# Kernel tuning notes

Measured on AMD Instinct MI355X. Metric: run time of the kernel, lower is better.

## Reference

```python
import jax, jax.numpy as jnp
import numpy as np
from math import sqrt

D_MODEL = 1024
N_HEADS = 16
FFN = 4096
B, N = 2, 2048
EPS = 1e-5


def _layernorm(x, g, b):
    mu = jnp.mean(x, -1, keepdims=True)
    var = jnp.mean((x - mu) ** 2, -1, keepdims=True)
    return (x - mu) * jax.lax.rsqrt(var + EPS) * g + b


def setup_inputs() -> dict:
    key = jax.random.key(0)
    ks = jax.random.split(key, 12)
    s = 1.0 / sqrt(D_MODEL)
    sf = 1.0 / sqrt(FFN)
    inp = {
        "tgt": jax.random.normal(ks[0], (B, N, D_MODEL), jnp.float32),
        # True = masked. Causal: query i may attend to keys j <= i.
        "tgt_mask": jnp.triu(jnp.ones((N, N), jnp.bool_), k=1),
        "tgt_key_pad_mask": jnp.zeros((B, N), jnp.bool_),
        "Wq": jax.random.uniform(ks[1], (D_MODEL, D_MODEL), jnp.float32, -s, s),
        "Wk": jax.random.uniform(ks[2], (D_MODEL, D_MODEL), jnp.float32, -s, s),
        "Wv": jax.random.uniform(ks[3], (D_MODEL, D_MODEL), jnp.float32, -s, s),
        "Wo": jax.random.uniform(ks[4], (D_MODEL, D_MODEL), jnp.float32, -s, s),
        "bo": jax.random.uniform(ks[5], (D_MODEL,), jnp.float32, -s, s),
        "W1": jax.random.uniform(ks[6], (FFN, D_MODEL), jnp.float32, -s, s),
        "b1": jax.random.uniform(ks[7], (FFN,), jnp.float32, -s, s),
        "W2": jax.random.uniform(ks[8], (D_MODEL, FFN), jnp.float32, -sf, sf),
        "b2": jax.random.uniform(ks[9], (D_MODEL,), jnp.float32, -sf, sf),
        "g1": jnp.ones((D_MODEL,), jnp.float32),
        "beta1": jnp.zeros((D_MODEL,), jnp.float32),
        "g2": jnp.ones((D_MODEL,), jnp.float32),
        "beta2": jnp.zeros((D_MODEL,), jnp.float32),
    }
    return inp


def _mha(x, tgt_mask, pad_mask, Wq, Wk, Wv, Wo, bo):
    b, n, d = x.shape
    dk = d // N_HEADS
    q = (x @ Wq.T).reshape(b, n, N_HEADS, dk).transpose(0, 2, 1, 3)  # bhnd
    k = (x @ Wk.T).reshape(b, n, N_HEADS, dk).transpose(0, 2, 1, 3)
    v = (x @ Wv.T).reshape(b, n, N_HEADS, dk).transpose(0, 2, 1, 3)
    scores = jnp.einsum("bhqd,bhkd->bhqk", q, k) / sqrt(dk)
    mask = tgt_mask[None, None, :, :] | pad_mask[:, None, None, :]
    scores = jnp.where(mask, -jnp.inf, scores)
    att = jax.nn.softmax(scores, axis=-1)
    out = jnp.einsum("bhqk,bhkd->bhqd", att, v).transpose(0, 2, 1, 3).reshape(b, n, d)
    return out @ Wo.T + bo


def reference(tgt, tgt_mask, tgt_key_pad_mask, Wq, Wk, Wv, Wo, bo,
              W1, b1, W2, b2, g1, beta1, g2, beta2):
    # PostNorm logic (pre_norm=False), dropout=0 (eval)
    h = _mha(tgt, tgt_mask, tgt_key_pad_mask, Wq, Wk, Wv, Wo, bo)
    x = _layernorm(tgt + h, g1, beta1)
    m = jax.nn.gelu(x @ W1.T + b1, approximate=True) @ W2.T + b2
    return _layernorm(x + m, g2, beta2)
```

## Files before the change

kernel.cpp:

```cpp
#include <hip/hip_runtime.h>


#define DEV __device__ __forceinline__

typedef __attribute__((ext_vector_type(4)))  float f32x4;
typedef __attribute__((ext_vector_type(16))) float f32x16;
typedef __attribute__((ext_vector_type(8)))  short s16x8;

static constexpr int Bb   = 2;
static constexpr int NN   = 2048;
static constexpr int DM   = 1024;
static constexpr int HH   = 16;
static constexpr int DK   = 64;
static constexpr int FF   = 4096;
static constexpr int ROWS = Bb * NN;

#define AS1(p) ((const __attribute__((address_space(1))) void*)(p))
#define AS3(p) ((__attribute__((address_space(3))) void*)(p))

DEV unsigned short f2bf(float f) {
  unsigned u = __float_as_uint(f);
  u += 0x7fff + ((u >> 16) & 1);
  return (unsigned short)(u >> 16);
}
DEV float fexp2(float x) {
  float r;
  asm("v_exp_f32 %0, %1" : "=v"(r) : "v"(x));
  return r;
}
DEV unsigned cvtpk(float lo, float hi) {
  unsigned r;
  asm("v_cvt_pk_bf16_f32 %0, %1, %2" : "=v"(r) : "v"(lo), "v"(hi));
  return r;
}

__global__ __launch_bounds__(256) void k_cast(const float* __restrict__ in,
                                              ushort* __restrict__ out, int n4) {
  int i = blockIdx.x * 256 + threadIdx.x;
  if (i >= n4) return;
  float4 v = reinterpret_cast<const float4*>(in)[i];
  ushort4 o;
  o.x = f2bf(v.x); o.y = f2bf(v.y); o.z = f2bf(v.z); o.w = f2bf(v.w);
  reinterpret_cast<ushort4*>(out)[i] = o;
}

template <int EPI, int BN, bool QKV>
__global__ __launch_bounds__(256) void k_gemm(
    const ushort* __restrict__ A, const ushort* __restrict__ Bt,
    const float* __restrict__ bias, const float* __restrict__ resid,
    ushort* __restrict__ Cb, float* __restrict__ Cf,
    int K, int nbx) {
  __shared__ ushort As[2][128][32];
  __shared__ ushort Bs[2][BN][32];

  const int t = threadIdx.x;
  const int lane = t & 63, w = t >> 6;
  const int lr = lane & 15, lg = lane >> 4;
  const int lrow = lane >> 2, lc8 = (lane & 3) * 8;

  const int nwg = gridDim.x;
  const int bid = blockIdx.x;
  const int q8 = nwg >> 3, r8 = nwg & 7;
  const int xcd = bid & 7, lin = bid >> 3;
  const int wg = (xcd < r8 ? xcd * (q8 + 1) : r8 * (q8 + 1) + (xcd - r8) * q8) + lin;
  const int band = wg / (4 * nbx);
  const int inn  = wg % (4 * nbx);
  const int by = band * 4 + (inn & 3);
  const int bx = inn >> 2;

  const int bRow = by * 128;
  const int bCol = bx * BN;

  constexpr int NW = BN / 32;
  const int wRow = (w >> 1) * 64, wCol = (w & 1) * (BN / 2);

  const f32x4 zero = {0.f, 0.f, 0.f, 0.f};
  f32x4 acc[4][NW];
#pragma unroll
  for (int m = 0; m < 4; ++m)
#pragma unroll
    for (int n = 0; n < NW; ++n) acc[m][n] = zero;

  auto stage = [&](int buf, int kt) {
#pragma unroll
    for (int i = 0; i < 2; ++i) {
      int rr = w * 32 + i * 16;
      __builtin_amdgcn_global_load_lds(
          AS1(A + (size_t)(bRow + rr + lrow) * K + kt + lc8),
          AS3(&As[buf][rr][0]), 16, 0, 0);
    }
#pragma unroll
    for (int i = 0; i < BN / 64; ++i) {
      int rr = w * (BN / 4) + i * 16;
      __builtin_amdgcn_global_load_lds(
          AS1(Bt + (size_t)(bCol + rr + lrow) * K + kt + lc8),
          AS3(&Bs[buf][rr][0]), 16, 0, 0);
    }
  };

  stage(0, 0);
  const int nk = K / 32;
  for (int tt = 0; tt < nk; ++tt) {
    const int cur = tt & 1;
    __syncthreads();
    if (tt + 1 < nk) stage(cur ^ 1, (tt + 1) * 32);

    s16x8 af[4], bfr[NW];
#pragma unroll
    for (int m = 0; m < 4; ++m)
      af[m] = *reinterpret_cast<const s16x8*>(&As[cur][wRow + m * 16 + lr][lg * 8]);
#pragma unroll
    for (int n = 0; n < NW; ++n)
      bfr[n] = *reinterpret_cast<const s16x8*>(&Bs[cur][wCol + n * 16 + lr][lg * 8]);
#pragma unroll
    for (int m = 0; m < 4; ++m)
#pragma unroll
      for (int n = 0; n < NW; ++n)
        acc[m][n] = __builtin_amdgcn_mfma_f32_16x16x32_bf16(af[m], bfr[n], acc[m][n], 0, 0, 0);
  }

  ushort* CbOut = Cb;
  int colBase = bCol, Ncols = nbx * BN, third = 0;
  if (QKV) {
    third = bCol >> 10;
    CbOut = Cb + (size_t)third * ROWS * DM;
    colBase = bCol & 1023;
    Ncols = DM;
  }
#pragma unroll
  for (int m = 0; m < 4; ++m) {
    int gr = bRow + wRow + m * 16 + lg * 4;
#pragma unroll
    for (int n = 0; n < NW; ++n) {
      int gc = colBase + wCol + n * 16 + lr;
      float bv = (EPI == 1 || EPI == 2) ? bias[gc] : 0.0f;
#pragma unroll
      for (int r = 0; r < 4; ++r) {
        int nr = gr + r;
        float v = acc[m][n][r] + bv;
        if (EPI == 2) {
          size_t idx = (size_t)nr * Ncols + gc;
          Cf[idx] = v + resid[idx];
        } else if (EPI == 1) {
          size_t idx = (size_t)nr * Ncols + gc;
          float u = v + 0.044715f * v * v * v;
          float g = v / (1.0f + __expf(-1.5957691216057308f * u));
          CbOut[idx] = f2bf(g);
        } else {
          int gcs = gc;
          if (QKV && third == 1)
            gcs = (gc & ~63) | ((gc ^ ((nr & 7) << 3)) & 63);
          CbOut[(size_t)nr * Ncols + gcs] = f2bf(v);
        }
      }
    }
  }
}

__global__ __launch_bounds__(256) void k_vt(const ushort* __restrict__ V,
                                            ushort* __restrict__ vT) {
  __shared__ ushort Ls[64][72];
  const int t = threadIdx.x;
  const int n0 = blockIdx.x * 64;
  const int bh = blockIdx.y;
  const int b = bh >> 4, h = bh & 15;
  const int n = t >> 2;
#pragma unroll
  for (int half = 0; half < 2; ++half) {
    int c8 = ((t & 3) + half * 4) * 8;
    int4 v = *reinterpret_cast<const int4*>(
        V + ((size_t)(b * NN + n0 + n)) * DM + h * DK + c8);
    *reinterpret_cast<int4*>(&Ls[n][c8]) = v;
  }
  __syncthreads();
  const int d = t >> 2;
#pragma unroll
  for (int half = 0; half < 2; ++half) {
    int c = (t & 3) + half * 4;
    ushort tmp[8];
#pragma unroll
    for (int j = 0; j < 8; ++j) tmp[j] = Ls[c * 8 + j][d];
    size_t out = ((size_t)bh * DK + d) * NN + n0 + ((c ^ (d & 7)) * 8);
    *reinterpret_cast<int4*>(vT + out) = *reinterpret_cast<const int4*>(tmp);
  }
}

template <int WB>
__global__ __launch_bounds__(256) void k_ln(const float* __restrict__ in,
                                            const float* __restrict__ g,
                                            const float* __restrict__ bta,
                                            float* __restrict__ outf,
                                            ushort* __restrict__ outb) {
  const int row = blockIdx.x;
  const int t = threadIdx.x;
  float4 v = reinterpret_cast<const float4*>(in + (size_t)row * DM)[t];
  float s1 = v.x + v.y + v.z + v.w;
  float s2 = v.x * v.x + v.y * v.y + v.z * v.z + v.w * v.w;
#pragma unroll
  for (int m = 32; m; m >>= 1) {
    s1 += __shfl_xor(s1, m, 64);
    s2 += __shfl_xor(s2, m, 64);
  }
  __shared__ float red[2][4];
  if ((t & 63) == 0) { red[0][t >> 6] = s1; red[1][t >> 6] = s2; }
  __syncthreads();
  s1 = red[0][0] + red[0][1] + red[0][2] + red[0][3];
  s2 = red[1][0] + red[1][1] + red[1][2] + red[1][3];
  const float mu = s1 * (1.0f / DM);
  const float var = s2 * (1.0f / DM) - mu * mu;
  const float rstd = rsqrtf(var + 1e-5f);
  float4 gv = reinterpret_cast<const float4*>(g)[t];
  float4 bv = reinterpret_cast<const float4*>(bta)[t];
  float4 o;
  o.x = (v.x - mu) * rstd * gv.x + bv.x;
  o.y = (v.y - mu) * rstd * gv.y + bv.y;
  o.z = (v.z - mu) * rstd * gv.z + bv.z;
  o.w = (v.w - mu) * rstd * gv.w + bv.w;
  reinterpret_cast<float4*>(outf + (size_t)row * DM)[t] = o;
  if (WB) {
    ushort4 ob;
    ob.x = f2bf(o.x); ob.y = f2bf(o.y); ob.z = f2bf(o.z); ob.w = f2bf(o.w);
    reinterpret_cast<ushort4*>(outb + (size_t)row * DM)[t] = ob;
  }
}

__global__ __launch_bounds__(256) void k_attn(const ushort* __restrict__ Q,
                                              const ushort* __restrict__ Kb,
                                              const ushort* __restrict__ vT,
                                              ushort* __restrict__ O) {
  __shared__ ushort Ks[2][64 * 64];
  __shared__ ushort Vs[2][64 * 64];

  const int t = threadIdx.x;
  const int qi = (NN / 128 - 1) - (int)blockIdx.x;
  const int bh = blockIdx.y;
  const int lane = t & 63, wid = t >> 6;
  const int l31 = lane & 31, hi = lane >> 5;
  const int q0w = qi * 128 + wid * 32;
  const size_t base = (size_t)bh * NN * DM / HH * HH;
  const size_t qbase = ((size_t)(bh >> 4) * NN) * DM + (bh & 15) * DK;
  const size_t vbase = (size_t)bh * DK * NN;
  (void)base;

  const float C = 0.18033688011112043f;

  s16x8 qf[4];
#pragma unroll
  for (int c = 0; c < 4; ++c)
    qf[c] = *reinterpret_cast<const s16x8*>(Q + qbase + (size_t)(q0w + l31) * DM + c * 16 + hi * 8);

  float mrun = -1e30f, lrun = 0.f, negcm = 1e30f;
  f32x16 accO[2];
#pragma unroll
  for (int dt = 0; dt < 2; ++dt)
#pragma unroll
    for (int r = 0; r < 16; ++r) accO[dt][r] = 0.f;

  auto stage = [&](int buf, int kt) {
    const int kk = kt * 64;
#pragma unroll
    for (int i = 0; i < 2; ++i) {
      int row0 = wid * 16 + i * 8;
      __builtin_amdgcn_global_load_lds(
          AS1(Kb + qbase + (size_t)(kk + row0 + (lane >> 3)) * DM + (lane & 7) * 8),
          AS3(&Ks[buf][row0 * 64]), 16, 0, 0);
      __builtin_amdgcn_global_load_lds(
          AS1(vT + vbase + (size_t)(row0 + (lane >> 3)) * NN + kk + (lane & 7) * 8),
          AS3(&Vs[buf][row0 * 64]), 16, 0, 0);
    }
  };

  const int nkt = 2 * qi + 2;
  stage(0, 0);
  for (int kt = 0; kt < nkt; ++kt) {
    const int cur = kt & 1;
    const int kk = kt * 64;
    __syncthreads();
    if (kt + 1 < nkt) stage(cur ^ 1, kt + 1);

    if (kk <= q0w + 31) {
      const char* KsB = (const char*)Ks[cur];
      const char* VsB = (const char*)Vs[cur];
      const bool diag = (kk + 64 > q0w);
      const int nsub = (kk + 32 <= q0w + 31) ? 2 : 1;

      f32x16 st[2];
#pragma unroll
      for (int sub = 0; sub < 2; ++sub) {
        if (sub >= nsub) break;
#pragma unroll
        for (int r = 0; r < 16; ++r) st[sub][r] = 0.f;
        const int row = sub * 32 + l31;
        const int swz = (row & 7) << 4;
#pragma unroll
        for (int c = 0; c < 4; ++c) {
          s16x8 kf = *reinterpret_cast<const s16x8*>(KsB + row * 128 + ((c * 32 + hi * 16) ^ swz));
          st[sub] = __builtin_amdgcn_mfma_f32_32x32x16_bf16(kf, qf[c], st[sub], 0, 0, 0);
        }
      }

      const int q = q0w + l31;
      float p[32];
#pragma unroll
      for (int sub = 0; sub < 2; ++sub) {
        if (sub >= nsub) break;
#pragma unroll
        for (int r = 0; r < 16; ++r) {
          float v = st[sub][r];
          if (diag) {
            int kl = sub * 32 + (r & 3) + 8 * (r >> 2) + 4 * hi;
            if (kk + kl > q) v = -1e30f;
          }
          p[sub * 16 + r] = v;
        }
      }
      float a[16];
#pragma unroll
      for (int i = 0; i < 16; ++i) a[i] = (nsub == 2) ? fmaxf(p[i], p[i + 16]) : p[i];
#pragma unroll
      for (int s = 8; s; s >>= 1)
#pragma unroll
        for (int i = 0; i < 8; ++i) if (i < s) a[i] = fmaxf(a[i], a[i + s]);
      float rm = fmaxf(a[0], __shfl_xor(a[0], 32, 64));

      if (__any(rm > mrun)) {
        const float mn = fmaxf(mrun, rm);
        const float alpha = fexp2(C * (mrun - mn));
        mrun = mn;
        negcm = -C * mn;
        lrun *= alpha;
#pragma unroll
        for (int dt = 0; dt < 2; ++dt) accO[dt] *= alpha;
      }

#pragma unroll
      for (int sub = 0; sub < 2; ++sub) {
        if (sub >= nsub) break;
#pragma unroll
        for (int i = 0; i < 16; ++i)
          p[sub * 16 + i] = fexp2(fmaf(p[sub * 16 + i], C, negcm));
      }
#pragma unroll
      for (int i = 0; i < 16; ++i) a[i] = (nsub == 2) ? (p[i] + p[i + 16]) : p[i];
#pragma unroll
      for (int s = 8; s; s >>= 1)
#pragma unroll
        for (int i = 0; i < 8; ++i) if (i < s) a[i] += a[i + s];
      lrun += a[0] + __shfl_xor(a[0], 32, 64);

      s16x8 pf[4];
#pragma unroll
      for (int sub = 0; sub < 2; ++sub) {
        if (sub >= nsub) break;
#pragma unroll
        for (int half = 0; half < 2; ++half) {
          const float* pp = &p[sub * 16 + half * 8];
          unsigned X0 = cvtpk(pp[0], pp[1]);
          unsigned X1 = cvtpk(pp[2], pp[3]);
          unsigned Y0 = cvtpk(pp[4], pp[5]);
          unsigned Y1 = cvtpk(pp[6], pp[7]);
          asm volatile("v_permlane32_swap_b32 %0, %1" : "+v"(X0), "+v"(Y0));
          asm volatile("v_permlane32_swap_b32 %0, %1" : "+v"(X1), "+v"(Y1));
          union { unsigned u[4]; s16x8 v; } uu;
          uu.u[0] = X0; uu.u[1] = X1; uu.u[2] = Y0; uu.u[3] = Y1;
          pf[sub * 2 + half] = uu.v;
        }
      }

#pragma unroll
      for (int dt = 0; dt < 2; ++dt) {
        const int d = dt * 32 + l31;
        const int vswz = (d & 7) << 4;
#pragma unroll
        for (int kc = 0; kc < 4; ++kc) {
          if (kc >= nsub * 2) break;
          s16x8 vf = *reinterpret_cast<const s16x8*>(VsB + d * 128 + ((kc * 32 + hi * 16) ^ vswz));
          accO[dt] = __builtin_amdgcn_mfma_f32_32x32x16_bf16(vf, pf[kc], accO[dt], 0, 0, 0);
        }
      }
    }
  }

  const int q = q0w + l31;
  const float inv = 1.0f / lrun;
#pragma unroll
  for (int dt = 0; dt < 2; ++dt)
#pragma unroll
    for (int rg = 0; rg < 4; ++rg) {
      int d0 = 8 * rg + 4 * hi + 32 * dt;
      ushort4 ov;
      ov.x = f2bf(accO[dt][rg * 4 + 0] * inv);
      ov.y = f2bf(accO[dt][rg * 4 + 1] * inv);
      ov.z = f2bf(accO[dt][rg * 4 + 2] * inv);
      ov.w = f2bf(accO[dt][rg * 4 + 3] * inv);
      *reinterpret_cast<ushort4*>(O + qbase + (size_t)q * DM + d0) = ov;
    }
}

extern "C" void kernel_launch(void* const* d_in, const int* in_sizes, int n_in,
                              void* d_out, int out_size, void* d_ws, size_t ws_size,
                              hipStream_t stream) {
  const float* tgt = (const float*)d_in[0];
  const float* Wq  = (const float*)d_in[3];
  const float* Wk  = (const float*)d_in[4];
  const float* Wv  = (const float*)d_in[5];
  const float* Wo  = (const float*)d_in[6];
  const float* bo  = (const float*)d_in[7];
  const float* W1  = (const float*)d_in[8];
  const float* b1  = (const float*)d_in[9];
  const float* W2  = (const float*)d_in[10];
  const float* b2  = (const float*)d_in[11];
  const float* g1  = (const float*)d_in[12];
  const float* be1 = (const float*)d_in[13];
  const float* g2  = (const float*)d_in[14];
  const float* be2 = (const float*)d_in[15];

  char* ws = (char*)d_ws;
  size_t off = 0;
  auto alloc = [&](size_t bytes) {
    void* p = ws + off;
    off += (bytes + 255) & ~(size_t)255;
    return p;
  };
  ushort* xb   = (ushort*)alloc((size_t)ROWS * DM * 2);
  ushort* wqb  = (ushort*)alloc((size_t)DM * DM * 2);
  ushort* wkb  = (ushort*)alloc((size_t)DM * DM * 2);
  ushort* wvb  = (ushort*)alloc((size_t)DM * DM * 2);
  ushort* wob  = (ushort*)alloc((size_t)DM * DM * 2);
  ushort* w1b  = (ushort*)alloc((size_t)FF * DM * 2);
  ushort* w2b  = (ushort*)alloc((size_t)DM * FF * 2);
  ushort* qbuf = (ushort*)alloc((size_t)ROWS * DM * 2);
  ushort* kbuf = (ushort*)alloc((size_t)ROWS * DM * 2);
  ushort* vbuf = (ushort*)alloc((size_t)ROWS * DM * 2);
  ushort* vtb  = (ushort*)alloc((size_t)ROWS * DM * 2);
  ushort* atnb = (ushort*)alloc((size_t)ROWS * DM * 2);
  float*  h1   = (float*)alloc((size_t)ROWS * DM * 4);
  float*  x1f  = (float*)alloc((size_t)ROWS * DM * 4);
  ushort* x1b  = (ushort*)alloc((size_t)ROWS * DM * 2);
  ushort* t1b  = (ushort*)alloc((size_t)ROWS * FF * 2);
  (void)ws_size; (void)in_sizes; (void)n_in; (void)out_size;
  (void)wkb; (void)wvb; (void)kbuf;

  auto cast = [&](const float* src, ushort* dst, size_t n) {
    int n4 = (int)(n / 4);
    k_cast<<<dim3((n4 + 255) / 256), 256, 0, stream>>>(src, dst, n4);
  };
  cast(tgt, xb, (size_t)ROWS * DM);
  cast(Wq, wqb, (size_t)DM * DM);
  cast(Wk, wkb, (size_t)DM * DM);
  cast(Wv, wvb, (size_t)DM * DM);
  cast(Wo, wob, (size_t)DM * DM);
  cast(W1, w1b, (size_t)FF * DM);
  cast(W2, w2b, (size_t)DM * FF);

  dim3 blk(256);
  k_gemm<0, 128, true><<<dim3(24 * 32), blk, 0, stream>>>(
      xb, wqb, nullptr, nullptr, qbuf, nullptr, DM, 24);

  k_vt<<<dim3(NN / 64, Bb * HH), blk, 0, stream>>>(vbuf, vtb);

  k_attn<<<dim3(NN / 128, Bb * HH), blk, 0, stream>>>(qbuf, kbuf, vtb, atnb);

  k_gemm<2, 64, false><<<dim3(16 * 32), blk, 0, stream>>>(
      atnb, wob, bo, tgt, nullptr, h1, DM, 16);
  k_ln<1><<<dim3(ROWS), blk, 0, stream>>>(h1, g1, be1, x1f, x1b);

  k_gemm<1, 128, false><<<dim3(32 * 32), blk, 0, stream>>>(
      x1b, w1b, b1, nullptr, t1b, nullptr, DM, 32);
  float* z = h1;
  k_gemm<2, 64, false><<<dim3(16 * 32), blk, 0, stream>>>(
      t1b, w2b, b2, x1f, nullptr, z, FF, 16);
  k_ln<0><<<dim3(ROWS), blk, 0, stream>>>(z, g2, be2, (float*)d_out, nullptr);
}
```

Baseline: 305.3 us.

## Fuse weight casts into one launch, remap attention blocks per XCD, add setprio

```diff
diff --git a/kernel.cpp b/kernel.cpp
--- a/kernel.cpp
+++ b/kernel.cpp
@@ -34,14 +34,29 @@
   return r;
 }
 
-__global__ __launch_bounds__(256) void k_cast(const float* __restrict__ in,
-                                              ushort* __restrict__ out, int n4) {
-  int i = blockIdx.x * 256 + threadIdx.x;
-  if (i >= n4) return;
-  float4 v = reinterpret_cast<const float4*>(in)[i];
+__global__ __launch_bounds__(256) void k_cast7(
+    const float* __restrict__ tgt, const float* __restrict__ Wq,
+    const float* __restrict__ Wk, const float* __restrict__ Wv,
+    const float* __restrict__ Wo, const float* __restrict__ W1,
+    const float* __restrict__ W2,
+    ushort* __restrict__ xb, ushort* __restrict__ wqb,
+    ushort* __restrict__ w1b, ushort* __restrict__ w2b) {
+  const int i = blockIdx.x * 256 + threadIdx.x;
+  constexpr int S0 = 1048576;
+  constexpr int S1 = 262144;
+  const float4* src;
+  ushort* dstp;
+  if (i < S0)               { src = (const float4*)tgt + i;            dstp = xb  + (size_t)i * 4; }
+  else if (i < S0 + S1)     { src = (const float4*)Wq + (i - S0);      dstp = wqb + (size_t)(i - S0) * 4; }
+  else if (i < S0 + 2 * S1) { src = (const float4*)Wk + (i - S0 - S1); dstp = wqb + (size_t)(i - S0) * 4; }
+  else if (i < S0 + 3 * S1) { src = (const float4*)Wv + (i - S0 - 2 * S1); dstp = wqb + (size_t)(i - S0) * 4; }
+  else if (i < S0 + 4 * S1) { src = (const float4*)Wo + (i - S0 - 3 * S1); dstp = wqb + (size_t)(i - S0) * 4; }
+  else if (i < 3 * S0)      { src = (const float4*)W1 + (i - 2 * S0);  dstp = w1b + (size_t)(i - 2 * S0) * 4; }
+  else                      { src = (const float4*)W2 + (i - 3 * S0);  dstp = w2b + (size_t)(i - 3 * S0) * 4; }
+  float4 v = *src;
   ushort4 o;
   o.x = f2bf(v.x); o.y = f2bf(v.y); o.z = f2bf(v.z); o.w = f2bf(v.w);
-  reinterpret_cast<ushort4*>(out)[i] = o;
+  *reinterpret_cast<ushort4*>(dstp) = o;
 }
 
 template <int EPI, int BN, bool QKV>
@@ -232,15 +247,15 @@
   __shared__ ushort Vs[2][64 * 64];
 
   const int t = threadIdx.x;
-  const int qi = (NN / 128 - 1) - (int)blockIdx.x;
-  const int bh = blockIdx.y;
+  const int bid = blockIdx.x;
+  const int xcd = bid & 7, j = bid >> 3;
+  const int bh = xcd * 4 + (j >> 4);
+  const int qi = 15 - (j & 15);
   const int lane = t & 63, wid = t >> 6;
   const int l31 = lane & 31, hi = lane >> 5;
   const int q0w = qi * 128 + wid * 32;
-  const size_t base = (size_t)bh * NN * DM / HH * HH;
   const size_t qbase = ((size_t)(bh >> 4) * NN) * DM + (bh & 15) * DK;
   const size_t vbase = (size_t)bh * DK * NN;
-  (void)base;
 
   const float C = 0.18033688011112043f;
 
@@ -285,6 +300,7 @@
       const int nsub = (kk + 32 <= q0w + 31) ? 2 : 1;
 
       f32x16 st[2];
+      __builtin_amdgcn_s_setprio(1);
 #pragma unroll
       for (int sub = 0; sub < 2; ++sub) {
         if (sub >= nsub) break;
@@ -298,6 +314,7 @@
           st[sub] = __builtin_amdgcn_mfma_f32_32x32x16_bf16(kf, qf[c], st[sub], 0, 0, 0);
         }
       }
+      __builtin_amdgcn_s_setprio(0);
 
       const int q = q0w + l31;
       float p[32];
@@ -353,8 +370,8 @@
       for (int sub = 0; sub < 2; ++sub) {
         if (sub >= nsub) break;
 #pragma unroll
-        for (int half = 0; half < 2; ++half) {
-          const float* pp = &p[sub * 16 + half * 8];
+        for (int hf = 0; hf < 2; ++hf) {
+          const float* pp = &p[sub * 16 + hf * 8];
           unsigned X0 = cvtpk(pp[0], pp[1]);
           unsigned X1 = cvtpk(pp[2], pp[3]);
           unsigned Y0 = cvtpk(pp[4], pp[5]);
@@ -363,10 +380,11 @@
           asm volatile("v_permlane32_swap_b32 %0, %1" : "+v"(X1), "+v"(Y1));
           union { unsigned u[4]; s16x8 v; } uu;
           uu.u[0] = X0; uu.u[1] = X1; uu.u[2] = Y0; uu.u[3] = Y1;
-          pf[sub * 2 + half] = uu.v;
+          pf[sub * 2 + hf] = uu.v;
         }
       }
 
+      __builtin_amdgcn_s_setprio(1);
 #pragma unroll
       for (int dt = 0; dt < 2; ++dt) {
         const int d = dt * 32 + l31;
@@ -378,6 +396,7 @@
           accO[dt] = __builtin_amdgcn_mfma_f32_32x32x16_bf16(vf, pf[kc], accO[dt], 0, 0, 0);
         }
       }
+      __builtin_amdgcn_s_setprio(0);
     }
   }
 
@@ -441,25 +460,16 @@
   (void)ws_size; (void)in_sizes; (void)n_in; (void)out_size;
   (void)wkb; (void)wvb; (void)kbuf;
 
-  auto cast = [&](const float* src, ushort* dst, size_t n) {
-    int n4 = (int)(n / 4);
-    k_cast<<<dim3((n4 + 255) / 256), 256, 0, stream>>>(src, dst, n4);
-  };
-  cast(tgt, xb, (size_t)ROWS * DM);
-  cast(Wq, wqb, (size_t)DM * DM);
-  cast(Wk, wkb, (size_t)DM * DM);
-  cast(Wv, wvb, (size_t)DM * DM);
-  cast(Wo, wob, (size_t)DM * DM);
-  cast(W1, w1b, (size_t)FF * DM);
-  cast(W2, w2b, (size_t)DM * FF);
-
   dim3 blk(256);
+  k_cast7<<<dim3(16384), blk, 0, stream>>>(tgt, Wq, Wk, Wv, Wo, W1, W2,
+                                           xb, wqb, w1b, w2b);
+
   k_gemm<0, 128, true><<<dim3(24 * 32), blk, 0, stream>>>(
       xb, wqb, nullptr, nullptr, qbuf, nullptr, DM, 24);
 
   k_vt<<<dim3(NN / 64, Bb * HH), blk, 0, stream>>>(vbuf, vtb);
 
-  k_attn<<<dim3(NN / 128, Bb * HH), blk, 0, stream>>>(qbuf, kbuf, vtb, atnb);
+  k_attn<<<dim3(512), blk, 0, stream>>>(qbuf, kbuf, vtb, atnb);
 
   k_gemm<2, 64, false><<<dim3(16 * 32), blk, 0, stream>>>(
       atnb, wob, bo, tgt, nullptr, h1, DM, 16);
```

Measured after the change: 290.0 us. 1.05x faster.
